# Kernel tuning notes

Hardware: AMD Instinct MI355X
Metric: run time of the kernel (lower is better)

## Reference

```python
import jax, jax.numpy as jnp
import numpy as np

S, E, H, T = 8192, 100, 768, 7  # seq_len, embed_dim, per-dir hidden, tagset


def setup_inputs() -> dict:
    key = jax.random.key(0)
    ks = jax.random.split(key, 16)
    s = 0.05
    return {
        "sentence": jax.random.normal(ks[0], (S, 1, E), dtype=jnp.float32),
        # forward-direction LSTM params (PyTorch gate order i,f,g,o)
        "w_ih_f": jax.random.normal(ks[1], (4 * H, E), dtype=jnp.float32) * s,
        "w_hh_f": jax.random.normal(ks[2], (4 * H, H), dtype=jnp.float32) * s,
        "b_ih_f": jnp.zeros((4 * H,), jnp.float32),
        "b_hh_f": jnp.zeros((4 * H,), jnp.float32),
        # backward-direction LSTM params
        "w_ih_b": jax.random.normal(ks[3], (4 * H, E), dtype=jnp.float32) * s,
        "w_hh_b": jax.random.normal(ks[4], (4 * H, H), dtype=jnp.float32) * s,
        "b_ih_b": jnp.zeros((4 * H,), jnp.float32),
        "b_hh_b": jnp.zeros((4 * H,), jnp.float32),
        # random initial states, as in init_hidden() (shape (2,1,H): dir, batch, H)
        "h0": jax.random.normal(ks[5], (2, 1, H), dtype=jnp.float32),
        "c0": jax.random.normal(ks[6], (2, 1, H), dtype=jnp.float32),
        # hidden2tag linear
        "w_tag": jax.random.normal(ks[7], (T, 2 * H), dtype=jnp.float32) * s,
        "b_tag": jnp.zeros((T,), jnp.float32),
        # CRF params
        "transitions": jax.random.normal(ks[8], (T, T), dtype=jnp.float32) * 0.1,
        "start_trans": jax.random.normal(ks[9], (T,), dtype=jnp.float32) * 0.1,
        "end_trans": jax.random.normal(ks[10], (T,), dtype=jnp.float32) * 0.1,
    }


def _lstm_dir(x, w_ih, w_hh, b_ih, b_hh, h0, c0):
    """Single-direction LSTM. x: (S,E); returns hidden states (S,H)."""
    xp = x @ w_ih.T + b_ih  # (S, 4H) input projection, one big GEMM

    def step(carry, xt):
        h, c = carry
        g = xt + h @ w_hh.T + b_hh
        i, f, gg, o = jnp.split(g, 4)
        i = jax.nn.sigmoid(i)
        f = jax.nn.sigmoid(f)
        gg = jnp.tanh(gg)
        o = jax.nn.sigmoid(o)
        c = f * c + i * gg
        h = o * jnp.tanh(c)
        return (h, c), h

    _, hs = jax.lax.scan(step, (h0, c0), xp)
    return hs


def reference(sentence, w_ih_f, w_hh_f, b_ih_f, b_hh_f,
              w_ih_b, w_hh_b, b_ih_b, b_hh_b, h0, c0,
              w_tag, b_tag, transitions, start_trans, end_trans):
    x = sentence[:, 0, :]  # (S, E), batch of 1
    hf = _lstm_dir(x, w_ih_f, w_hh_f, b_ih_f, b_hh_f, h0[0, 0], c0[0, 0])
    hb = _lstm_dir(x[::-1], w_ih_b, w_hh_b, b_ih_b, b_hh_b, h0[1, 0], c0[1, 0])[::-1]
    lstm_out = jnp.concatenate([hf, hb], axis=-1)  # (S, 2H)
    feats = lstm_out @ w_tag.T + b_tag             # (S, T) emission scores

    # CRF forward algorithm (log-partition) -- sequential DP over tiny tagset
    alpha0 = start_trans + feats[0]

    def crf_step(alpha, emit):
        alpha = jax.nn.logsumexp(alpha[:, None] + transitions + emit[None, :], axis=0)
        return alpha, None

    alpha, _ = jax.lax.scan(crf_step, alpha0, feats[1:])
    return jax.nn.logsumexp(alpha + end_trans)  # scalar log Z
```

## Files before the change

kernel.cpp:

```cpp
#include <hip/hip_runtime.h>
#include <stdint.h>

#define S_LEN 8192
#define E_DIM 100
#define H_DIM 768
#define NTAG 7
#define G4 3072
#define NBLK 96
#define NCHUNK 128
#define POLL_LIMIT 150000

typedef unsigned short u16;
typedef unsigned long long u64;
typedef __attribute__((ext_vector_type(4))) float f4v;

__device__ int g_isbf16;

__device__ __forceinline__ u16 f2bf(float f) {
    union { float f; unsigned u; } v; v.f = f;
    unsigned b = v.u;
    unsigned r = (b + 0x7FFFu + ((b >> 16) & 1u)) >> 16;
    return (u16)r;
}
__device__ __forceinline__ float bf2f(u16 u) {
    union { unsigned u; float f; } v; v.u = ((unsigned)u) << 16;
    return v.f;
}
__device__ __forceinline__ float getv(const void* p, size_t i, int isbf) {
    return isbf ? bf2f(((const u16*)p)[i]) : ((const float*)p)[i];
}
__device__ __forceinline__ float sigm(float x) {
    return __builtin_amdgcn_rcpf(1.0f + __expf(-x));
}
__device__ __forceinline__ float ftanh(float x) {
    return 2.0f * __builtin_amdgcn_rcpf(1.0f + __expf(-2.0f * x)) - 1.0f;
}

__global__ void detect(const void* x) {
    __shared__ int cnt;
    if (threadIdx.x == 0) cnt = 0;
    __syncthreads();
    unsigned v = ((const u16*)x)[2 * threadIdx.x];
    int e = (v >> 7) & 0xFF;
    if (e >= 110 && e <= 132) atomicAdd(&cnt, 1);
    __syncthreads();
    if (threadIdx.x == 0) g_isbf16 = (cnt >= 100) ? 1 : 0;
}

__global__ void prep(const void* bihf, const void* bhhf,
                     const void* bihb, const void* bhhb,
                     const void* h0, const void* c0,
                     float* __restrict__ cst, float* __restrict__ bias,
                     u64* __restrict__ slots) {
    const int isbf = g_isbf16;
    int i = blockIdx.x * blockDim.x + threadIdx.x;
    if (i < G4) {
        bias[i]      = getv(bihf, i, isbf) + getv(bhhf, i, isbf);
        bias[G4 + i] = getv(bihb, i, isbf) + getv(bhhb, i, isbf);
    }
    if (i < 2 * H_DIM) cst[i] = getv(c0, i, isbf);
    if (i < 384) {
        unsigned pf = (unsigned)f2bf(getv(h0, 2 * i, isbf))
                    | ((unsigned)f2bf(getv(h0, 2 * i + 1, isbf)) << 16);
        unsigned pb = (unsigned)f2bf(getv(h0, H_DIM + 2 * i, isbf))
                    | ((unsigned)f2bf(getv(h0, H_DIM + 2 * i + 1, isbf)) << 16);
        slots[i]        = (u64)pf;
        slots[768 + i]  = (u64)pb;
        slots[384 + i]  = 0xFFFFFFFF00000000ull;
        slots[1152 + i] = 0xFFFFFFFF00000000ull;
    }
}

__global__ __launch_bounds__(256, 1) void lstm_persist(
        const void* x,
        const void* wihf, const void* whhf,
        const void* wihb, const void* whhb,
        u16* __restrict__ hfseq, u16* __restrict__ hbseq,
        float* __restrict__ cstate, const float* __restrict__ biasv,
        u64* __restrict__ slots, int* __restrict__ bail) {
    const int isbf = g_isbf16;
    const int bid = blockIdx.x;
    const int dir = (bid >= NBLK) ? 1 : 0;
    const int blk = bid - dir * NBLK;
    const int tid = threadIdx.x;
    const int wave = tid >> 6, lane = tid & 63;
    const int seg = tid & 7;
    const int row = tid >> 3;
    const int gamma = row & 3;
    const int uloc = row >> 2;
    const int u = blk * 8 + uloc;
    const size_t grow = (size_t)(gamma * H_DIM + u);
    u16* hseq = dir ? hbseq : hfseq;
    u64* myslots = slots + (size_t)dir * 768;
    const void* Wih = dir ? wihb : wihf;
    const void* Whh = dir ? whhb : whhf;

    __shared__ float sh[1600];

    float whh[96], wih[13];
    if (isbf) {
        const unsigned* p = (const unsigned*)((const u16*)Whh + grow * H_DIM + seg * 96);
        #pragma unroll
        for (int i = 0; i < 48; ++i) {
            unsigned q = p[i];
            whh[2 * i] = bf2f((u16)q); whh[2 * i + 1] = bf2f((u16)(q >> 16));
        }
        const unsigned* px = (const unsigned*)((const u16*)Wih + grow * E_DIM + seg * 12);
        #pragma unroll
        for (int i = 0; i < 6; ++i) {
            unsigned q = px[i];
            wih[2 * i] = bf2f((u16)q); wih[2 * i + 1] = bf2f((u16)(q >> 16));
        }
        wih[12] = (seg < 4) ? bf2f(((const u16*)Wih)[grow * E_DIM + 96 + seg]) : 0.f;
    } else {
        const float* p = (const float*)Whh + grow * H_DIM + seg * 96;
        #pragma unroll
        for (int i = 0; i < 96; ++i) whh[i] = p[i];
        const float* px = (const float*)Wih + grow * E_DIM + seg * 12;
        #pragma unroll
        for (int i = 0; i < 12; ++i) wih[i] = px[i];
        wih[12] = (seg < 4) ? ((const float*)Wih)[grow * E_DIM + 96 + seg] : 0.f;
    }
    const float bias_r = biasv[dir * G4 + grow];
    const int uhalf = blk * 8 + wave * 2 + (lane >> 5);
    float cst = cstate[dir * H_DIM + uhalf];

    const bool has2 = (tid < 128);
    const int k0 = 2 * tid;
    const int o0 = (k0 / 96) * 100 + (k0 % 96);
    const int k1 = 512 + 2 * tid;
    const int o1 = (k1 / 96) * 100 + (k1 % 96);
    const int pubslot = blk * 4 + wave;

    float    xf[13];
    unsigned xu[6];
    u16      xt16 = 0;
    auto load_x = [&](int t) {
        const int sx = dir ? (S_LEN - 1 - t) : t;
        if (isbf) {
            const unsigned* xr = (const unsigned*)((const u16*)x + (size_t)sx * E_DIM + seg * 12);
            #pragma unroll
            for (int i = 0; i < 6; ++i) xu[i] = xr[i];
            if (seg < 4) xt16 = ((const u16*)x)[(size_t)sx * E_DIM + 96 + seg];
        } else {
            const float* xr = (const float*)x + (size_t)sx * E_DIM + seg * 12;
            #pragma unroll
            for (int i = 0; i < 12; ++i) xf[i] = xr[i];
            xf[12] = (seg < 4) ? ((const float*)x)[(size_t)sx * E_DIM + 96 + seg] : 0.f;
        }
    };
    auto fma_x = [&]() -> float {
        float ax = 0.f;
        if (isbf) {
            #pragma unroll
            for (int i = 0; i < 6; ++i) {
                unsigned q = xu[i];
                ax += wih[2 * i] * bf2f((u16)q) + wih[2 * i + 1] * bf2f((u16)(q >> 16));
            }
            if (seg < 4) ax += wih[12] * bf2f(xt16);
        } else {
            #pragma unroll
            for (int i = 0; i < 12; ++i) ax += wih[i] * xf[i];
            ax += wih[12] * xf[12];
        }
        return ax;
    };

    load_x(0);

    for (int t = 0; t < S_LEN; ++t) {
        float ax = fma_x();

        u64 v0 = 0, v1 = 0;
        {
            u64* buf = myslots + (size_t)(t & 1) * 384;
            const unsigned tgt = (unsigned)t;
            const u64 pass = ((u64)tgt) << 32;
            u64 a0 = __hip_atomic_load(&buf[tid], __ATOMIC_RELAXED,
                                       __HIP_MEMORY_SCOPE_AGENT);
            u64 a1 = has2 ? __hip_atomic_load(&buf[256 + tid], __ATOMIC_RELAXED,
                                              __HIP_MEMORY_SCOPE_AGENT) : pass;
            int polls = 0;
            for (;;) {
                u64 b0 = __hip_atomic_load(&buf[tid], __ATOMIC_RELAXED,
                                           __HIP_MEMORY_SCOPE_AGENT);
                u64 b1 = has2 ? __hip_atomic_load(&buf[256 + tid], __ATOMIC_RELAXED,
                                                  __HIP_MEMORY_SCOPE_AGENT) : pass;
                if (((unsigned)(a0 >> 32) == tgt) && ((unsigned)(a1 >> 32) == tgt)) {
                    v0 = a0; v1 = a1; break;
                }
                u64 c0 = __hip_atomic_load(&buf[tid], __ATOMIC_RELAXED,
                                           __HIP_MEMORY_SCOPE_AGENT);
                u64 c1 = has2 ? __hip_atomic_load(&buf[256 + tid], __ATOMIC_RELAXED,
                                                  __HIP_MEMORY_SCOPE_AGENT) : pass;
                if (((unsigned)(b0 >> 32) == tgt) && ((unsigned)(b1 >> 32) == tgt)) {
                    v0 = b0; v1 = b1; break;
                }
                a0 = c0; a1 = c1;
                polls += 2;
                if ((polls & 63) == 0) {
                    if (__hip_atomic_load(bail, __ATOMIC_RELAXED,
                                          __HIP_MEMORY_SCOPE_AGENT)) {
                        v0 = b0; v1 = b1; break;
                    }
                    if (polls > POLL_LIMIT) {
                        __hip_atomic_store(bail, 1, __ATOMIC_RELAXED,
                                           __HIP_MEMORY_SCOPE_AGENT);
                        v0 = b0; v1 = b1; break;
                    }
                    __builtin_amdgcn_s_sleep(1);
                }
            }
        }

        float* shb = sh + (t & 1) * 800;
        {
            unsigned p0 = (unsigned)v0;
            shb[o0]     = bf2f((u16)p0);
            shb[o0 + 1] = bf2f((u16)(p0 >> 16));
            if (has2) {
                unsigned p1 = (unsigned)v1;
                shb[o1]     = bf2f((u16)p1);
                shb[o1 + 1] = bf2f((u16)(p1 >> 16));
            }
        }
        __syncthreads();

        load_x((t + 1 < S_LEN) ? (t + 1) : t);

        const float* hs = shb + seg * 100;
        float a0 = 0.f, a1 = 0.f, a2 = 0.f, a3 = 0.f;
        #pragma unroll
        for (int i = 0; i < 24; ++i) {
            f4v hv = *(const f4v*)(hs + 4 * i);
            a0 += whh[4 * i]     * hv.x;
            a1 += whh[4 * i + 1] * hv.y;
            a2 += whh[4 * i + 2] * hv.z;
            a3 += whh[4 * i + 3] * hv.w;
        }
        float acc = ax + (a0 + a1) + (a2 + a3);
        acc += __shfl_xor(acc, 1);
        acc += __shfl_xor(acc, 2);
        acc += __shfl_xor(acc, 4);
        float g = acc + bias_r;

        const int base = lane & 32;
        float gi = __shfl(g, base + 0);
        float gf = __shfl(g, base + 8);
        float gg = __shfl(g, base + 16);
        float go = __shfl(g, base + 24);
        float ii = sigm(gi), ff = sigm(gf), gt = ftanh(gg), oo = sigm(go);
        float c = ff * cst + ii * gt;
        cst = c;
        float h = oo * ftanh(c);

        {
            float hodd = __shfl(h, 32);
            if (lane == 0) {
                unsigned pk = (unsigned)f2bf(h) | ((unsigned)f2bf(hodd) << 16);
                u64 sv = (((u64)(unsigned)(t + 1)) << 32) | (u64)pk;
                __hip_atomic_store(&myslots[(size_t)((t + 1) & 1) * 384 + pubslot],
                                   sv, __ATOMIC_RELAXED, __HIP_MEMORY_SCOPE_AGENT);
                __hip_atomic_store(
                    &((unsigned*)(hseq + (size_t)(t + 1) * H_DIM))[pubslot],
                    pk, __ATOMIC_RELAXED, __HIP_MEMORY_SCOPE_AGENT);
            }
        }
    }
}

__global__ __launch_bounds__(256) void feats_kernel(const u16* __restrict__ hfseq,
                                                    const u16* __restrict__ hbseq,
                                                    const void* w_tag, const void* b_tag,
                                                    float* __restrict__ feats) {
    const int isbf = g_isbf16;
    const int wave = threadIdx.x >> 6, lane = threadIdx.x & 63;
    const int s = blockIdx.x * 4 + wave;
    if (s >= S_LEN) return;
    const u16* hf = hfseq + (size_t)(s + 1) * H_DIM;
    const u16* hb = hbseq + (size_t)(S_LEN - s) * H_DIM;
    float hv[12], hbv[12];
    #pragma unroll
    for (int i = 0; i < 12; ++i) {
        hv[i]  = bf2f(hf[lane + 64 * i]);
        hbv[i] = bf2f(hb[lane + 64 * i]);
    }
    float myf = 0.f;
    for (int j = 0; j < NTAG; ++j) {
        const size_t wr = (size_t)j * (2 * H_DIM);
        float d = 0.f;
        #pragma unroll
        for (int i = 0; i < 12; ++i)
            d += hv[i] * getv(w_tag, wr + lane + 64 * i, isbf)
               + hbv[i] * getv(w_tag, wr + H_DIM + lane + 64 * i, isbf);
        #pragma unroll
        for (int m = 1; m < 64; m <<= 1) d += __shfl_xor(d, m);
        if (lane == j) myf = d + getv(b_tag, j, isbf);
    }
    if (lane < NTAG) feats[(size_t)s * NTAG + lane] = myf;
}

__global__ void crf_chunks(const void* trans,
                           const float* __restrict__ feats,
                           float* __restrict__ cmats) {
    const int isbf = g_isbf16;
    const int c = blockIdx.x;
    const int lane = threadIdx.x;
    const bool act = lane < 49;
    const int i = act ? (lane / 7) : 0;
    const int j = lane % 7;
    float tc[7];
    #pragma unroll
    for (int k = 0; k < 7; ++k) tc[k] = getv(trans, k * 7 + j, isbf);
    float R = (act && (lane / 7) == j) ? 0.f : -1e30f;
    int s0 = 1 + c * 64;
    int s1 = s0 + 64; if (s1 > S_LEN) s1 = S_LEN;
    for (int t = s0; t < s1; ++t) {
        float fj = feats[t * NTAG + j];
        float r[7];
        #pragma unroll
        for (int k = 0; k < 7; ++k) r[k] = __shfl(R, i * 7 + k) + tc[k];
        float m = r[0];
        #pragma unroll
        for (int k = 1; k < 7; ++k) m = fmaxf(m, r[k]);
        float sum = 0.f;
        #pragma unroll
        for (int k = 0; k < 7; ++k) sum += __expf(r[k] - m);
        R = m + __logf(sum) + fj;
    }
    if (act) cmats[c * 49 + lane] = R;
}

__global__ void crf_final(const void* start_t, const void* end_t,
                          const float* __restrict__ feats,
                          const float* __restrict__ cmats,
                          void* __restrict__ out) {
    const int isbf = g_isbf16;
    const int lane = threadIdx.x;
    const int j = (lane < 7) ? lane : 0;
    float alpha = (lane < 7) ? (getv(start_t, lane, isbf) + feats[lane]) : -1e30f;
    for (int c = 0; c < NCHUNK; ++c) {
        float r[7];
        #pragma unroll
        for (int i = 0; i < 7; ++i)
            r[i] = __shfl(alpha, i) + cmats[c * 49 + i * 7 + j];
        float m = r[0];
        #pragma unroll
        for (int i = 1; i < 7; ++i) m = fmaxf(m, r[i]);
        float sum = 0.f;
        #pragma unroll
        for (int i = 0; i < 7; ++i) sum += __expf(r[i] - m);
        float na = m + __logf(sum);
        alpha = (lane < 7) ? na : -1e30f;
    }
    float v = (lane < 7) ? (alpha + getv(end_t, lane, isbf)) : -1e30f;
    float m = v;
    #pragma unroll
    for (int d = 1; d < 8; d <<= 1) m = fmaxf(m, __shfl_xor(m, d));
    float s = __expf(v - m);
    #pragma unroll
    for (int d = 1; d < 8; d <<= 1) s += __shfl_xor(s, d);
    if (lane == 0) {
        float r = m + __logf(s);
        if (isbf) ((u16*)out)[0] = f2bf(r);
        else      ((float*)out)[0] = r;
    }
}

extern "C" void kernel_launch(void* const* d_in, const int* in_sizes, int n_in,
                              void* d_out, int out_size, void* d_ws, size_t ws_size,
                              hipStream_t stream) {
    const void* sentence = d_in[0];
    const void* w_ih_f   = d_in[1];
    const void* w_hh_f   = d_in[2];
    const void* b_ih_f   = d_in[3];
    const void* b_hh_f   = d_in[4];
    const void* w_ih_b   = d_in[5];
    const void* w_hh_b   = d_in[6];
    const void* b_ih_b   = d_in[7];
    const void* b_hh_b   = d_in[8];
    const void* h0       = d_in[9];
    const void* c0       = d_in[10];
    const void* w_tag    = d_in[11];
    const void* b_tag    = d_in[12];
    const void* trans    = d_in[13];
    const void* start_t  = d_in[14];
    const void* end_t    = d_in[15];
    (void)in_sizes; (void)n_in; (void)out_size; (void)ws_size;

    char* ws = (char*)d_ws;
    size_t o = 0;
    auto take = [&](size_t bytes) -> char* {
        char* p = ws + o;
        o += (bytes + 255) & ~(size_t)255;
        return p;
    };
    u16*   hfseq  = (u16*)take((size_t)(S_LEN + 1) * H_DIM * 2);
    u16*   hbseq  = (u16*)take((size_t)(S_LEN + 1) * H_DIM * 2);
    float* cstate = (float*)take((size_t)2 * H_DIM * 4);
    float* biasv  = (float*)take((size_t)2 * G4 * 4);
    float* featsb = (float*)take((size_t)S_LEN * NTAG * 4);
    float* cmats  = (float*)take((size_t)NCHUNK * 49 * 4);
    u64*   slots  = (u64*)take((size_t)2 * 2 * 384 * 8);
    int*   bail   = (int*)take((size_t)256 * 4);

    detect<<<1, 128, 0, stream>>>(sentence);
    prep<<<12, 256, 0, stream>>>(b_ih_f, b_hh_f, b_ih_b, b_hh_b, h0, c0,
                                 cstate, biasv, slots);
    (void)hipMemsetAsync(bail, 0, 4, stream);

    lstm_persist<<<2 * NBLK, 256, 0, stream>>>(sentence,
                                               w_ih_f, w_hh_f, w_ih_b, w_hh_b,
                                               hfseq, hbseq, cstate, biasv,
                                               slots, bail);

    feats_kernel<<<S_LEN / 4, 256, 0, stream>>>(hfseq, hbseq, w_tag, b_tag, featsb);
    crf_chunks<<<NCHUNK, 64, 0, stream>>>(trans, featsb, cmats);
    crf_final<<<1, 64, 0, stream>>>(start_t, end_t, featsb, cmats, d_out);
}
```

Baseline: 16.22 ms.

## Pipeline cross-block h-state polling with inline-asm cache-bypassing loads and wave-uniform checks

Rewrites the per-step spin-wait that reads the previous step's hidden state from the global slot buffer. It now issues double-buffered global_load_dwordx2 with sc0 sc1 through inline asm and waits on partial vmcnt, so a new poll is always in flight. Readiness is checked per wave with __all, and the slot-to-thread mapping is rearranged so each wave reads its own contiguous slots. The aim is lower handoff latency between the persistent blocks. The cost is hand-managed vmcnt accounting and a different backoff schedule, which could break ordering or hurt under contention.

After: 15.86 ms. -2.2%, faster.

```diff
diff --git a/kernel.cpp b/kernel.cpp
--- a/kernel.cpp
+++ b/kernel.cpp
@@ -70,6 +70,16 @@
         slots[1152 + i] = 0xFFFFFFFF00000000ull;
     }
 }
+
+#define PISSUE(A, B)                                                     \
+    asm volatile("global_load_dwordx2 %0, %2, off sc0 sc1\n\t"           \
+                 "global_load_dwordx2 %1, %3, off sc0 sc1"               \
+                 : "=&v"(A), "=&v"(B) : "v"(pa), "v"(pb) : "memory")
+#define PWAIT2(A, B)                                                     \
+    asm volatile("s_waitcnt vmcnt(2)" : "+v"(A), "+v"(B))
+#define PDRAIN4(A, B, C, D)                                              \
+    asm volatile("s_waitcnt vmcnt(0)"                                    \
+                 : "+v"(A), "+v"(B), "+v"(C), "+v"(D))
 
 __global__ __launch_bounds__(256, 1) void lstm_persist(
         const void* x,
@@ -125,11 +135,10 @@
     const int uhalf = blk * 8 + wave * 2 + (lane >> 5);
     float cst = cstate[dir * H_DIM + uhalf];
 
-    const bool has2 = (tid < 128);
-    const int k0 = 2 * tid;
-    const int o0 = (k0 / 96) * 100 + (k0 % 96);
-    const int k1 = 512 + 2 * tid;
-    const int o1 = (k1 / 96) * 100 + (k1 % 96);
+    const int sA = wave * 96 + lane;
+    const int sB = (lane < 32) ? (wave * 96 + 64 + lane) : sA;
+    const int oA = (2 * wave + (lane >= 48)) * 100 + 2 * lane - ((lane >= 48) ? 96 : 0);
+    const int oB = (2 * wave + 1) * 100 + 32 + 2 * lane;
     const int pubslot = blk * 4 + wave;
 
     float    xf[13];
@@ -171,64 +180,70 @@
     for (int t = 0; t < S_LEN; ++t) {
         float ax = fma_x();
 
-        u64 v0 = 0, v1 = 0;
+        u64 va = 0, vb = 0;
         {
-            u64* buf = myslots + (size_t)(t & 1) * 384;
+            const u64* buf = myslots + (size_t)(t & 1) * 384;
+            const u64* pa = buf + sA;
+            const u64* pb = buf + sB;
             const unsigned tgt = (unsigned)t;
-            const u64 pass = ((u64)tgt) << 32;
-            u64 a0 = __hip_atomic_load(&buf[tid], __ATOMIC_RELAXED,
+            u64 a0, b0, a1, b1;
+            int polls = 0;
+            bool found = false;
+            asm volatile("s_waitcnt vmcnt(0)" ::: "memory");
+            for (;;) {
+                PISSUE(a0, b0);
+                for (int it = 0; it < 32; ++it) {
+                    PISSUE(a1, b1);
+                    PWAIT2(a0, b0);
+                    if (__all(((unsigned)(a0 >> 32) == tgt) &
+                              ((unsigned)(b0 >> 32) == tgt))) {
+                        va = a0; vb = b0; found = true; break;
+                    }
+                    PISSUE(a0, b0);
+                    PWAIT2(a1, b1);
+                    if (__all(((unsigned)(a1 >> 32) == tgt) &
+                              ((unsigned)(b1 >> 32) == tgt))) {
+                        va = a1; vb = b1; found = true; break;
+                    }
+                }
+                PDRAIN4(a0, b0, a1, b1);
+                if (found) break;
+                u64 f0 = __hip_atomic_load(&buf[sA], __ATOMIC_RELAXED,
+                                           __HIP_MEMORY_SCOPE_AGENT);
+                u64 f1 = __hip_atomic_load(&buf[sB], __ATOMIC_RELAXED,
+                                           __HIP_MEMORY_SCOPE_AGENT);
+                if (__all(((unsigned)(f0 >> 32) == tgt) &
+                          ((unsigned)(f1 >> 32) == tgt))) {
+                    va = f0; vb = f1; break;
+                }
+                polls += 64;
+                if (__hip_atomic_load(bail, __ATOMIC_RELAXED,
+                                      __HIP_MEMORY_SCOPE_AGENT)) {
+                    va = f0; vb = f1; break;
+                }
+                if (polls > POLL_LIMIT) {
+                    __hip_atomic_store(bail, 1, __ATOMIC_RELAXED,
                                        __HIP_MEMORY_SCOPE_AGENT);
-            u64 a1 = has2 ? __hip_atomic_load(&buf[256 + tid], __ATOMIC_RELAXED,
-                                              __HIP_MEMORY_SCOPE_AGENT) : pass;
-            int polls = 0;
-            for (;;) {
-                u64 b0 = __hip_atomic_load(&buf[tid], __ATOMIC_RELAXED,
-                                           __HIP_MEMORY_SCOPE_AGENT);
-                u64 b1 = has2 ? __hip_atomic_load(&buf[256 + tid], __ATOMIC_RELAXED,
-                                                  __HIP_MEMORY_SCOPE_AGENT) : pass;
-                if (((unsigned)(a0 >> 32) == tgt) && ((unsigned)(a1 >> 32) == tgt)) {
-                    v0 = a0; v1 = a1; break;
+                    va = f0; vb = f1; break;
                 }
-                u64 c0 = __hip_atomic_load(&buf[tid], __ATOMIC_RELAXED,
-                                           __HIP_MEMORY_SCOPE_AGENT);
-                u64 c1 = has2 ? __hip_atomic_load(&buf[256 + tid], __ATOMIC_RELAXED,
-                                                  __HIP_MEMORY_SCOPE_AGENT) : pass;
-                if (((unsigned)(b0 >> 32) == tgt) && ((unsigned)(b1 >> 32) == tgt)) {
-                    v0 = b0; v1 = b1; break;
-                }
-                a0 = c0; a1 = c1;
-                polls += 2;
-                if ((polls & 63) == 0) {
-                    if (__hip_atomic_load(bail, __ATOMIC_RELAXED,
-                                          __HIP_MEMORY_SCOPE_AGENT)) {
-                        v0 = b0; v1 = b1; break;
-                    }
-                    if (polls > POLL_LIMIT) {
-                        __hip_atomic_store(bail, 1, __ATOMIC_RELAXED,
-                                           __HIP_MEMORY_SCOPE_AGENT);
-                        v0 = b0; v1 = b1; break;
-                    }
-                    __builtin_amdgcn_s_sleep(1);
-                }
+                __builtin_amdgcn_s_sleep(2);
             }
-        }
-
-        float* shb = sh + (t & 1) * 800;
-        {
-            unsigned p0 = (unsigned)v0;
-            shb[o0]     = bf2f((u16)p0);
-            shb[o0 + 1] = bf2f((u16)(p0 >> 16));
-            if (has2) {
-                unsigned p1 = (unsigned)v1;
-                shb[o1]     = bf2f((u16)p1);
-                shb[o1 + 1] = bf2f((u16)(p1 >> 16));
+
+            float* shb = sh + (t & 1) * 800;
+            unsigned p0 = (unsigned)va;
+            shb[oA]     = bf2f((u16)p0);
+            shb[oA + 1] = bf2f((u16)(p0 >> 16));
+            if (lane < 32) {
+                unsigned p1 = (unsigned)vb;
+                shb[oB]     = bf2f((u16)p1);
+                shb[oB + 1] = bf2f((u16)(p1 >> 16));
             }
         }
         __syncthreads();
 
         load_x((t + 1 < S_LEN) ? (t + 1) : t);
 
-        const float* hs = shb + seg * 100;
+        const float* hs = sh + (t & 1) * 800 + seg * 100;
         float a0 = 0.f, a1 = 0.f, a2 = 0.f, a3 = 0.f;
         #pragma unroll
         for (int i = 0; i < 24; ++i) {
```
